# Kernel optimization log

Measured on AMD Instinct MI355X. Metric: run time of the kernel, lower is better.

Reference implementation:

```python
import jax, jax.numpy as jnp
import numpy as np

B, T, D, H = 32, 512, 512, 512  # batch, seq_len, emb dim, lstm_size
TAGS = (17, 9, 25, 13)


def _reverse_sequence(x, lengths):
    # tf.reverse_sequence semantics: reverse first `len` steps, keep the tail.
    t = jnp.arange(x.shape[1])
    idx = jnp.where(t[None, :] < lengths[:, None], lengths[:, None] - 1 - t[None, :], t[None, :])
    return jnp.take_along_axis(x, idx[:, :, None], axis=1)


def _lstm(x, W, b, lengths):
    # TF LSTMCell: kernel [D+H,4H], gate order (i, j, f, o), forget_bias=1.0.
    # dynamic_rnn: state copied through past seq_len, outputs zeroed past seq_len.
    Bx, Tx, _ = x.shape
    Hh = b.shape[-1] // 4
    xT = jnp.swapaxes(x, 0, 1)  # [T,B,D]
    mask = (jnp.arange(Tx)[:, None] < lengths[None, :]).astype(x.dtype)[:, :, None]  # [T,B,1]

    def step(carry, inp):
        c, h = carry
        xt, m = inp
        z = jnp.concatenate([xt, h], axis=-1) @ W + b  # [B,4H]
        i, j, f, o = jnp.split(z, 4, axis=-1)
        c_new = jax.nn.sigmoid(f + 1.0) * c + jax.nn.sigmoid(i) * jnp.tanh(j)
        h_new = jax.nn.sigmoid(o) * jnp.tanh(c_new)
        c = m * c_new + (1.0 - m) * c
        h = m * h_new + (1.0 - m) * h
        return (c, h), h * m

    init = (jnp.zeros((Bx, Hh), x.dtype), jnp.zeros((Bx, Hh), x.dtype))
    _, hs = jax.lax.scan(step, init, (xT, mask))
    return jnp.swapaxes(hs, 0, 1)  # [B,T,H]


def _bilstm(x, lengths, Wf, bf, Wb, bb):
    out_fw = _lstm(x, Wf, bf, lengths)
    x_rev = _reverse_sequence(x, lengths)
    out_bw = _reverse_sequence(_lstm(x_rev, Wb, bb, lengths), lengths)
    return jnp.concatenate([out_fw, out_bw], axis=2)  # [B,T,2H]


def setup_inputs() -> dict:
    key = jax.random.key(0)
    ks = jax.random.split(key, 12)
    s_in = 1.0 / np.sqrt(D + H)
    s_fc = 1.0 / np.sqrt(4 * H)
    inp = {
        'embedded_words': jax.random.normal(ks[0], (B, T, D), jnp.float32),
        'sentence_lengths': jax.random.randint(ks[1], (B,), 16, T + 1, jnp.int32),
        'W_fw': jax.random.normal(ks[2], (5, D + H, 4 * H), jnp.float32) * s_in,
        'b_fw': jnp.zeros((5, 4 * H), jnp.float32),
        'W_bw': jax.random.normal(ks[3], (5, D + H, 4 * H), jnp.float32) * s_in,
        'b_bw': jnp.zeros((5, 4 * H), jnp.float32),
    }
    for i, tg in enumerate(TAGS):
        inp[f'W{i+1}'] = jax.random.normal(ks[4 + i], (4 * H, tg), jnp.float32) * s_fc
        inp[f'b{i+1}'] = jnp.zeros((tg,), jnp.float32)
    return inp


def reference(embedded_words, sentence_lengths, W_fw, b_fw, W_bw, b_bw,
              W1, b1, W2, b2, W3, b3, W4, b4):
    # 5 independent BiLSTMs (task1..4 + shared) over the same input, vmapped over the stack axis.
    outs = jax.vmap(lambda wf, bf, wb, bb: _bilstm(embedded_words, sentence_lengths, wf, bf, wb, bb))(
        W_fw, b_fw, W_bw, b_bw)  # [5,B,T,2H]
    shared = outs[4]
    logits = []
    for i, (Wk, bk) in enumerate(((W1, b1), (W2, b2), (W3, b3), (W4, b4))):
        feat = jnp.concatenate([outs[i], shared], axis=2)  # [B,T,4H]; dropout = identity (inference)
        logits.append(jnp.einsum('btd,dk->btk', feat, Wk) + bk)
    # concatenate the 4 task logit heads along the tag axis: [B,T,sum(TAGS)]
    return jnp.concatenate(logits, axis=2)
```

## Files before the change

### kernel.cpp

```cpp
#include <hip/hip_runtime.h>
#include <cstdint>
#include <cstddef>

#define BB 32
#define TT 512
#define DD 512
#define HH 512
#define FOURH 2048
#define DIRS 10
#define HSZ ((size_t)DIRS * BB * HH)
#define LWPITCH 520
#define SMEM_REC (128 * LWPITCH * 2 + 2 * 2 * 4 * 4 * 64 * 4)

typedef unsigned short u16;
typedef __attribute__((ext_vector_type(8))) short short8;
typedef __attribute__((ext_vector_type(4))) float f32x4;

__device__ __forceinline__ u16 f2b(float f) {
    union { float f; unsigned u; } v; v.f = f;
    unsigned u = v.u;
    u = (u + 0x7FFFu + ((u >> 16) & 1u)) >> 16;
    return (u16)u;
}
__device__ __forceinline__ float b2f(u16 b) {
    union { unsigned u; float f; } v; v.u = ((unsigned)b) << 16;
    return v.f;
}
__device__ __forceinline__ float sigm(float x) { return 1.f / (1.f + __expf(-x)); }
__device__ __forceinline__ float tanh_(float x) { return 1.f - 2.f / (1.f + __expf(2.f * x)); }
__device__ __forceinline__ f32x4 fzero() { f32x4 z = {0.f, 0.f, 0.f, 0.f}; return z; }

__device__ __forceinline__ uint4 load_coh16(const u16* p) {
    uint4 r;
    asm volatile("global_load_dwordx4 %0, %1, off sc0 sc1"
                 : "=v"(r) : "v"(p) : "memory");
    return r;
}

__global__ void k_convx(const float* __restrict__ X, u16* __restrict__ XB) {
    int i = blockIdx.x * 256 + threadIdx.x;
    if (i >= (BB * TT * DD) / 4) return;
    float4 v = ((const float4*)X)[i];
    unsigned lo = (unsigned)f2b(v.x) | ((unsigned)f2b(v.y) << 16);
    unsigned hi = (unsigned)f2b(v.z) | ((unsigned)f2b(v.w) << 16);
    uint2 o; o.x = lo; o.y = hi;
    ((uint2*)XB)[i] = o;
}

__global__ void k_wt(const float* __restrict__ Wf, const float* __restrict__ Wb,
                     u16* __restrict__ WT) {
    int d = blockIdx.z, s = d >> 1;
    const float* src = (d & 1) ? Wb : Wf;
    __shared__ float tile[32][33];
    int tx = threadIdx.x & 31, ty = threadIdx.x >> 5;
    int kt = blockIdx.x, nt = blockIdx.y;
#pragma unroll
    for (int r = 0; r < 4; r++) {
        int k = kt * 32 + ty + r * 8, n = nt * 32 + tx;
        tile[ty + r * 8][tx] = src[((size_t)s * 1024 + k) * 2048 + n];
    }
    __syncthreads();
#pragma unroll
    for (int r = 0; r < 4; r++) {
        int n = nt * 32 + ty + r * 8, k = kt * 32 + tx;
        WT[((size_t)d * 2048 + n) * 1024 + k] = f2b(tile[tx][ty + r * 8]);
    }
}

__global__ void k_wbt(const float* W1, const float* W2, const float* W3, const float* W4,
                      const float* b1, const float* b2, const float* b3, const float* b4,
                      u16* __restrict__ WBT, float* __restrict__ B64) {
    int idx = blockIdx.x * 256 + threadIdx.x;
    const int off[4] = {0, 17, 26, 51};
    const int tg[4]  = {17, 9, 25, 13};
    if (idx < 64) {
        int c = idx;
        int ti = (c < 17) ? 0 : (c < 26) ? 1 : (c < 51) ? 2 : 3;
        const float* bbp[4] = {b1, b2, b3, b4};
        B64[c] = bbp[ti][c - off[ti]];
    }
    if (idx >= 64 * 5120) return;
    int c = idx / 5120, k = idx % 5120;
    int ti = (c < 17) ? 0 : (c < 26) ? 1 : (c < 51) ? 2 : 3;
    const float* Ws[4] = {W1, W2, W3, W4};
    int tag = c - off[ti];
    float v;
    if (k < 4096) {
        int i = k >> 10, kk = k & 1023;
        v = (i == ti) ? Ws[ti][(size_t)kk * tg[ti] + tag] : 0.f;
    } else {
        int kk = k - 4096;
        v = Ws[ti][(size_t)(1024 + kk) * tg[ti] + tag];
    }
    WBT[(size_t)c * 5120 + k] = f2b(v);
}

__global__ __launch_bounds__(512, 2) void k_rec(
    const u16* __restrict__ WT, const u16* __restrict__ XB,
    const float* __restrict__ bfw, const float* __restrict__ bbw,
    u16* __restrict__ Hbuf, float* __restrict__ Cst, u16* __restrict__ OUTS,
    const int* __restrict__ lens, unsigned* __restrict__ ctr)
{
    extern __shared__ char smem[];
    u16* lWx = (u16*)smem;
    float* red = (float*)(smem + 128 * LWPITCH * 2);

    int blk = blockIdx.x, d = blk >> 4, jj = blk & 15;
    int s = d >> 1, isbw = d & 1;
    int tid = threadIdx.x, w = tid >> 6, lane = tid & 63, quad = lane >> 4, l15 = lane & 15;
    int mtile = w & 1, nhalf = (w >> 1) & 1, khalf = w >> 2;

#pragma unroll
    for (int it = 0; it < 16; ++it) {
        int g16 = it * 512 + tid;
        int row = g16 >> 6, c = g16 & 63;
        int n = (row >> 5) * 512 + jj * 32 + (row & 31);
        const u16* src = WT + ((size_t)d * 2048 + n) * 1024 + c * 8;
        *(uint4*)(lWx + row * LWPITCH + c * 8) = *(const uint4*)src;
    }

    short8 Bf[8][4];
#pragma unroll
    for (int ks = 0; ks < 8; ks++) {
        int k0 = khalf * 256 + ks * 32;
#pragma unroll
        for (int g = 0; g < 4; g++) {
            int n = g * 512 + jj * 32 + nhalf * 16 + l15;
            Bf[ks][g] = *(const short8*)(WT + ((size_t)d * 2048 + n) * 1024 + 512 + k0 + quad * 8);
        }
    }

    int bA = mtile * 16 + l15;
    int lbA = lens[bA];
    int ug = jj * 32 + nhalf * 16 + l15;
    const float* bias = (isbw ? bbw : bfw) + (size_t)s * 2048;
    float c_reg[4], hprev[4], bv_r[4];
    int lb_r[4];
    if (khalf == 0) {
#pragma unroll
        for (int g = 0; g < 4; g++) bv_r[g] = bias[g * 512 + ug];
#pragma unroll
        for (int r = 0; r < 4; r++) {
            int b = mtile * 16 + quad * 4 + r;
            lb_r[r] = lens[b];
            c_reg[r] = Cst[((size_t)d * BB + b) * HH + ug];
            hprev[r] = b2f(Hbuf[(size_t)d * BB * HH + (size_t)b * HH + ug]);
        }
    }
    __syncthreads();

    for (int t = 0; t < TT; ++t) {
        const u16* hin = Hbuf + (size_t)(t & 1) * HSZ + (size_t)d * BB * HH;
        u16* hout      = Hbuf + (size_t)((t + 1) & 1) * HSZ + (size_t)d * BB * HH;

        int srcT = isbw ? ((t < lbA) ? (lbA - 1 - t) : t) : t;
        const u16* xrow = XB + ((size_t)bA * TT + srcT) * DD + khalf * 256;
        uint4 xraw[8];
#pragma unroll
        for (int ks = 0; ks < 8; ks++)
            xraw[ks] = *(const uint4*)(xrow + ks * 32 + quad * 8);

        uint4 araw[8];
#pragma unroll
        for (int ks = 0; ks < 8; ks++)
            araw[ks] = load_coh16(hin + (size_t)bA * HH + khalf * 256 + ks * 32 + quad * 8);

        f32x4 acc[4];
#pragma unroll
        for (int g = 0; g < 4; g++) acc[g] = fzero();

#pragma unroll
        for (int ks = 0; ks < 8; ks++) {
            short8 a = *(const short8*)(&xraw[ks]);
#pragma unroll
            for (int g = 0; g < 4; g++) {
                short8 bfr = *(const short8*)(lWx + (g * 32 + nhalf * 16 + l15) * LWPITCH
                                              + khalf * 256 + ks * 32 + quad * 8);
                acc[g] = __builtin_amdgcn_mfma_f32_16x16x32_bf16(a, bfr, acc[g], 0, 0, 0);
            }
        }

        asm volatile("s_waitcnt vmcnt(0)" ::: "memory");
#pragma unroll
        for (int ks = 0; ks < 8; ks++) {
            short8 a = *(const short8*)(&araw[ks]);
#pragma unroll
            for (int g = 0; g < 4; g++)
                acc[g] = __builtin_amdgcn_mfma_f32_16x16x32_bf16(a, Bf[ks][g], acc[g], 0, 0, 0);
        }

        if (khalf == 1) {
#pragma unroll
            for (int g = 0; g < 4; g++)
#pragma unroll
                for (int r = 0; r < 4; r++)
                    red[((((size_t)mtile * 2 + nhalf) * 4 + g) * 4 + r) * 64 + lane] = acc[g][r];
        }
        __syncthreads();
        if (khalf == 0) {
#pragma unroll
            for (int g = 0; g < 4; g++)
#pragma unroll
                for (int r = 0; r < 4; r++)
                    acc[g][r] += red[((((size_t)mtile * 2 + nhalf) * 4 + g) * 4 + r) * 64 + lane];

#pragma unroll
            for (int r = 0; r < 4; r++) {
                int b = mtile * 16 + quad * 4 + r;
                int lb = lb_r[r];
                float zi = acc[0][r] + bv_r[0];
                float zj = acc[1][r] + bv_r[1];
                float zf = acc[2][r] + bv_r[2];
                float zo = acc[3][r] + bv_r[3];
                float cn = sigm(zf + 1.f) * c_reg[r] + sigm(zi) * tanh_(zj);
                float hn = sigm(zo) * tanh_(cn);
                bool act = t < lb;
                if (act) c_reg[r] = cn;
                u16 hv = f2b(act ? hn : hprev[r]);
                hprev[r] = b2f(hv);
                __hip_atomic_store(&hout[(size_t)b * HH + ug], hv,
                                   __ATOMIC_RELAXED, __HIP_MEMORY_SCOPE_AGENT);
                int twr = isbw ? (act ? (lb - 1 - t) : t) : t;
                OUTS[(((size_t)s * BB + b) * TT + twr) * 1024 + isbw * 512 + ug] = f2b(act ? hn : 0.f);
            }
        }

        __syncthreads();
        if (tid == 0) {
            atomicAdd(ctr + d * 16, 1u);
            unsigned target = 16u * (unsigned)(t + 1);
            while (__hip_atomic_load(ctr + d * 16, __ATOMIC_RELAXED, __HIP_MEMORY_SCOPE_AGENT) < target)
                __builtin_amdgcn_s_sleep(1);
        }
        __syncthreads();
    }
}

__global__ __launch_bounds__(256) void k_head(
    const u16* __restrict__ OUTS, const u16* __restrict__ WBT,
    const float* __restrict__ B64, float* __restrict__ OUT)
{
    int tid = threadIdx.x, w = tid >> 6, lane = tid & 63, quad = lane >> 4, l15 = lane & 15;
    int mtile = blockIdx.x * 4 + w, r0 = mtile * 16;
    int row_a = r0 + l15, ba = row_a >> 9, ta = row_a & 511;
    f32x4 acc[4];
#pragma unroll
    for (int ni = 0; ni < 4; ni++) acc[ni] = fzero();

    for (int k0 = 0; k0 < 5120; k0 += 32) {
        int kidx = k0 + quad * 8;
        int blkk = kidx >> 10, kk = kidx & 1023;
        short8 a = *(const short8*)(OUTS + (((size_t)blkk * BB + ba) * TT + ta) * 1024 + kk);
#pragma unroll
        for (int ni = 0; ni < 4; ni++) {
            short8 bf = *(const short8*)(WBT + (size_t)(ni * 16 + l15) * 5120 + kidx);
            acc[ni] = __builtin_amdgcn_mfma_f32_16x16x32_bf16(a, bf, acc[ni], 0, 0, 0);
        }
    }
#pragma unroll
    for (int ni = 0; ni < 4; ni++) {
        int c = ni * 16 + l15;
        float bv = B64[c];
#pragma unroll
        for (int r = 0; r < 4; r++) {
            int row = r0 + quad * 4 + r;
            OUT[(size_t)row * 64 + c] = acc[ni][r] + bv;
        }
    }
}

extern "C" void kernel_launch(void* const* d_in, const int* in_sizes, int n_in,
                              void* d_out, int out_size, void* d_ws, size_t ws_size,
                              hipStream_t stream) {
    const float* X   = (const float*)d_in[0];
    const int* lens  = (const int*)d_in[1];
    const float* Wf  = (const float*)d_in[2];
    const float* bf_ = (const float*)d_in[3];
    const float* Wb  = (const float*)d_in[4];
    const float* bb_ = (const float*)d_in[5];
    const float* W1  = (const float*)d_in[6];
    const float* b1  = (const float*)d_in[7];
    const float* W2  = (const float*)d_in[8];
    const float* b2  = (const float*)d_in[9];
    const float* W3  = (const float*)d_in[10];
    const float* b3  = (const float*)d_in[11];
    const float* W4  = (const float*)d_in[12];
    const float* b4  = (const float*)d_in[13];

    char* ws = (char*)d_ws;
    size_t off = 0;
    auto take = [&](size_t bytes) { size_t o = off; off += (bytes + 255) & ~(size_t)255; return o; };
    size_t wtOff   = take((size_t)DIRS * 2048 * 1024 * 2);
    size_t xbOff   = take((size_t)BB * TT * DD * 2);
    size_t outsOff = take((size_t)5 * BB * TT * 1024 * 2);
    size_t hOff    = take((size_t)2 * HSZ * 2);
    size_t cOff    = take((size_t)HSZ * 4);
    size_t ctrOff  = take((size_t)DIRS * 16 * 4);
    size_t wbtOff  = take((size_t)64 * 5120 * 2);
    size_t b64Off  = take((size_t)64 * 4);

    u16* WT    = (u16*)(ws + wtOff);
    u16* XB    = (u16*)(ws + xbOff);
    u16* OUTS  = (u16*)(ws + outsOff);
    u16* Hbuf  = (u16*)(ws + hOff);
    float* Cst = (float*)(ws + cOff);
    unsigned* CTR = (unsigned*)(ws + ctrOff);
    u16* WBT   = (u16*)(ws + wbtOff);
    float* B64 = (float*)(ws + b64Off);

    hipMemsetAsync(ws + hOff, 0, wbtOff - hOff, stream);

    (void)hipFuncSetAttribute((const void*)k_rec,
                              hipFuncAttributeMaxDynamicSharedMemorySize, SMEM_REC);

    k_convx<<<8192, 256, 0, stream>>>(X, XB);
    k_wt<<<dim3(32, 64, 10), 256, 0, stream>>>(Wf, Wb, WT);
    k_wbt<<<1280, 256, 0, stream>>>(W1, W2, W3, W4, b1, b2, b3, b4, WBT, B64);

    k_rec<<<160, 512, SMEM_REC, stream>>>(WT, XB, bf_, bb_, Hbuf, Cst, OUTS, lens, CTR);

    k_head<<<256, 256, 0, stream>>>(OUTS, WBT, B64, (float*)d_out);
}
```

Baseline: 3.692 ms.

## Replace per-step grid barrier with per-wave producer flags and prefetch next x row

Swaps the per-direction atomic counter barrier (two block-wide syncs plus one spinning thread) for per-wave flag words. Each producing wave publishes its timestep after its h stores drain, and each consumer wave polls only the 32 flags covering the h slice it reads. The x input row for the next step is also prefetched at the end of each iteration, so that load overlaps the wait. This cuts the cost of the serial dependency at each timestep, but adds more polling traffic and depends on relaxed-store ordering after vmcnt(0).

```diff
diff --git a/kernel.cpp b/kernel.cpp
--- a/kernel.cpp
+++ b/kernel.cpp
@@ -33,6 +33,12 @@
 __device__ __forceinline__ uint4 load_coh16(const u16* p) {
     uint4 r;
     asm volatile("global_load_dwordx4 %0, %1, off sc0 sc1"
+                 : "=v"(r) : "v"(p) : "memory");
+    return r;
+}
+__device__ __forceinline__ uint4 load_p16(const u16* p) {
+    uint4 r;
+    asm volatile("global_load_dwordx4 %0, %1, off"
                  : "=v"(r) : "v"(p) : "memory");
     return r;
 }
@@ -99,7 +105,7 @@
     const u16* __restrict__ WT, const u16* __restrict__ XB,
     const float* __restrict__ bfw, const float* __restrict__ bbw,
     u16* __restrict__ Hbuf, float* __restrict__ Cst, u16* __restrict__ OUTS,
-    const int* __restrict__ lens, unsigned* __restrict__ ctr)
+    const int* __restrict__ lens, unsigned* __restrict__ flg)
 {
     extern __shared__ char smem[];
     u16* lWx = (u16*)smem;
@@ -147,23 +153,45 @@
             hprev[r] = b2f(Hbuf[(size_t)d * BB * HH + (size_t)b * HH + ug]);
         }
     }
+
+    unsigned* FLG = flg + d * 64;
+    const unsigned* myfl = FLG + khalf * 32;
+    int myflag = jj * 4 + mtile * 2 + nhalf;
+
     __syncthreads();
+
+    uint4 xraw[8];
+    {
+        int srcT = isbw ? (lbA - 1) : 0;
+        const u16* xrow = XB + ((size_t)bA * TT + srcT) * DD + khalf * 256;
+#pragma unroll
+        for (int ks = 0; ks < 8; ks++)
+            xraw[ks] = load_p16(xrow + ks * 32 + quad * 8);
+    }
 
     for (int t = 0; t < TT; ++t) {
         const u16* hin = Hbuf + (size_t)(t & 1) * HSZ + (size_t)d * BB * HH;
         u16* hout      = Hbuf + (size_t)((t + 1) & 1) * HSZ + (size_t)d * BB * HH;
 
-        int srcT = isbw ? ((t < lbA) ? (lbA - 1 - t) : t) : t;
-        const u16* xrow = XB + ((size_t)bA * TT + srcT) * DD + khalf * 256;
-        uint4 xraw[8];
-#pragma unroll
-        for (int ks = 0; ks < 8; ks++)
-            xraw[ks] = *(const uint4*)(xrow + ks * 32 + quad * 8);
+        if (t > 0) {
+            unsigned tgt = (unsigned)t;
+            for (;;) {
+                unsigned f = tgt;
+                if (lane < 32)
+                    f = __hip_atomic_load(myfl + lane, __ATOMIC_RELAXED,
+                                          __HIP_MEMORY_SCOPE_AGENT);
+                if (__all((int)(f >= tgt))) break;
+                __builtin_amdgcn_s_sleep(1);
+            }
+        }
 
         uint4 araw[8];
 #pragma unroll
         for (int ks = 0; ks < 8; ks++)
             araw[ks] = load_coh16(hin + (size_t)bA * HH + khalf * 256 + ks * 32 + quad * 8);
+
+        asm volatile("s_waitcnt vmcnt(8)" ::: "memory");
+        __builtin_amdgcn_sched_barrier(0);
 
         f32x4 acc[4];
 #pragma unroll
@@ -181,6 +209,7 @@
         }
 
         asm volatile("s_waitcnt vmcnt(0)" ::: "memory");
+        __builtin_amdgcn_sched_barrier(0);
 #pragma unroll
         for (int ks = 0; ks < 8; ks++) {
             short8 a = *(const short8*)(&araw[ks]);
@@ -189,6 +218,7 @@
                 acc[g] = __builtin_amdgcn_mfma_f32_16x16x32_bf16(a, Bf[ks][g], acc[g], 0, 0, 0);
         }
 
+        __syncthreads();
         if (khalf == 1) {
 #pragma unroll
             for (int g = 0; g < 4; g++)
@@ -223,16 +253,19 @@
                 int twr = isbw ? (act ? (lb - 1 - t) : t) : t;
                 OUTS[(((size_t)s * BB + b) * TT + twr) * 1024 + isbw * 512 + ug] = f2b(act ? hn : 0.f);
             }
-        }
-
-        __syncthreads();
-        if (tid == 0) {
-            atomicAdd(ctr + d * 16, 1u);
-            unsigned target = 16u * (unsigned)(t + 1);
-            while (__hip_atomic_load(ctr + d * 16, __ATOMIC_RELAXED, __HIP_MEMORY_SCOPE_AGENT) < target)
-                __builtin_amdgcn_s_sleep(1);
-        }
-        __syncthreads();
+            asm volatile("s_waitcnt vmcnt(0)" ::: "memory");
+            __builtin_amdgcn_sched_barrier(0);
+            if (lane == 0)
+                __hip_atomic_store(FLG + myflag, (unsigned)(t + 1),
+                                   __ATOMIC_RELAXED, __HIP_MEMORY_SCOPE_AGENT);
+        }
+
+        int tn = (t + 1 < TT) ? (t + 1) : (TT - 1);
+        int srcTn = isbw ? ((tn < lbA) ? (lbA - 1 - tn) : tn) : tn;
+        const u16* xrown = XB + ((size_t)bA * TT + srcTn) * DD + khalf * 256;
+#pragma unroll
+        for (int ks = 0; ks < 8; ks++)
+            xraw[ks] = load_p16(xrown + ks * 32 + quad * 8);
     }
 }
 
@@ -295,7 +328,7 @@
     size_t outsOff = take((size_t)5 * BB * TT * 1024 * 2);
     size_t hOff    = take((size_t)2 * HSZ * 2);
     size_t cOff    = take((size_t)HSZ * 4);
-    size_t ctrOff  = take((size_t)DIRS * 16 * 4);
+    size_t flgOff  = take((size_t)DIRS * 64 * 4);
     size_t wbtOff  = take((size_t)64 * 5120 * 2);
     size_t b64Off  = take((size_t)64 * 4);
 
@@ -304,7 +337,7 @@
     u16* OUTS  = (u16*)(ws + outsOff);
     u16* Hbuf  = (u16*)(ws + hOff);
     float* Cst = (float*)(ws + cOff);
-    unsigned* CTR = (unsigned*)(ws + ctrOff);
+    unsigned* FLG = (unsigned*)(ws + flgOff);
     u16* WBT   = (u16*)(ws + wbtOff);
     float* B64 = (float*)(ws + b64Off);
 
@@ -317,7 +350,7 @@
     k_wt<<<dim3(32, 64, 10), 256, 0, stream>>>(Wf, Wb, WT);
     k_wbt<<<1280, 256, 0, stream>>>(W1, W2, W3, W4, b1, b2, b3, b4, WBT, B64);
 
-    k_rec<<<160, 512, SMEM_REC, stream>>>(WT, XB, bf_, bb_, Hbuf, Cst, OUTS, lens, CTR);
+    k_rec<<<160, 512, SMEM_REC, stream>>>(WT, XB, bf_, bb_, Hbuf, Cst, OUTS, lens, FLG);
 
     k_head<<<256, 256, 0, stream>>>(OUTS, WBT, B64, (float*)d_out);
 }
```

Measured after the change: 4.041 ms. +9.5%, slower.

## Interleave fwd/bwd directions per block with per-block flag barriers

Applied to the files above, without the earlier changes.

Each block now owns 16 hidden units for both the forward and the backward direction of one stack and alternates between them within each time step. While one direction waits on its cross-block dependency, the other direction's work can proceed. The single atomic counter barrier is replaced by per-block step flags that a wavefront polls in parallel, and the other direction's flags are prefetched. The gate reduction and cell update are spread across all 512 threads with a padded LDS layout. The change adds complexity, a bounded spin loop, and a relaxed-ordering flag protocol that could race.

```diff
diff --git a/kernel.cpp b/kernel.cpp
--- a/kernel.cpp
+++ b/kernel.cpp
@@ -6,11 +6,11 @@
 #define TT 512
 #define DD 512
 #define HH 512
-#define FOURH 2048
 #define DIRS 10
 #define HSZ ((size_t)DIRS * BB * HH)
 #define LWPITCH 520
-#define SMEM_REC (128 * LWPITCH * 2 + 2 * 2 * 4 * 4 * 64 * 4)
+#define REDPITCH 66
+#define SMEM_REC (128 * LWPITCH * 2 + 64 * REDPITCH * 4)
 
 typedef unsigned short u16;
 typedef __attribute__((ext_vector_type(8))) short short8;
@@ -98,141 +98,155 @@
 __global__ __launch_bounds__(512, 2) void k_rec(
     const u16* __restrict__ WT, const u16* __restrict__ XB,
     const float* __restrict__ bfw, const float* __restrict__ bbw,
-    u16* __restrict__ Hbuf, float* __restrict__ Cst, u16* __restrict__ OUTS,
-    const int* __restrict__ lens, unsigned* __restrict__ ctr)
+    u16* __restrict__ Hbuf, u16* __restrict__ OUTS,
+    const int* __restrict__ lens, unsigned* __restrict__ flg)
 {
     extern __shared__ char smem[];
     u16* lWx = (u16*)smem;
     float* red = (float*)(smem + 128 * LWPITCH * 2);
 
-    int blk = blockIdx.x, d = blk >> 4, jj = blk & 15;
-    int s = d >> 1, isbw = d & 1;
+    int blk = blockIdx.x, s = blk >> 5, jj = blk & 31, d0 = s * 2;
     int tid = threadIdx.x, w = tid >> 6, lane = tid & 63, quad = lane >> 4, l15 = lane & 15;
-    int mtile = w & 1, nhalf = (w >> 1) & 1, khalf = w >> 2;
+    int gsel = w & 1, mtile = (w >> 1) & 1, khalf = w >> 2;
 
 #pragma unroll
     for (int it = 0; it < 16; ++it) {
         int g16 = it * 512 + tid;
         int row = g16 >> 6, c = g16 & 63;
-        int n = (row >> 5) * 512 + jj * 32 + (row & 31);
-        const u16* src = WT + ((size_t)d * 2048 + n) * 1024 + c * 8;
+        int dq = row >> 6, local = row & 63;
+        int n = (local >> 4) * 512 + jj * 16 + (local & 15);
+        const u16* src = WT + ((size_t)(d0 + dq) * 2048 + n) * 1024 + c * 8;
         *(uint4*)(lWx + row * LWPITCH + c * 8) = *(const uint4*)src;
     }
 
-    short8 Bf[8][4];
-#pragma unroll
-    for (int ks = 0; ks < 8; ks++) {
-        int k0 = khalf * 256 + ks * 32;
-#pragma unroll
-        for (int g = 0; g < 4; g++) {
-            int n = g * 512 + jj * 32 + nhalf * 16 + l15;
-            Bf[ks][g] = *(const short8*)(WT + ((size_t)d * 2048 + n) * 1024 + 512 + k0 + quad * 8);
-        }
-    }
+    short8 Bf[2][8][2];
+#pragma unroll
+    for (int dd = 0; dd < 2; dd++)
+#pragma unroll
+        for (int ks = 0; ks < 8; ks++)
+#pragma unroll
+            for (int gb = 0; gb < 2; gb++) {
+                int n = (gsel * 2 + gb) * 512 + jj * 16 + l15;
+                int k = 512 + khalf * 256 + ks * 32 + quad * 8;
+                Bf[dd][ks][gb] = *(const short8*)(WT + ((size_t)(d0 + dd) * 2048 + n) * 1024 + k);
+            }
 
     int bA = mtile * 16 + l15;
     int lbA = lens[bA];
-    int ug = jj * 32 + nhalf * 16 + l15;
-    const float* bias = (isbw ? bbw : bfw) + (size_t)s * 2048;
-    float c_reg[4], hprev[4], bv_r[4];
-    int lb_r[4];
-    if (khalf == 0) {
-#pragma unroll
-        for (int g = 0; g < 4; g++) bv_r[g] = bias[g * 512 + ug];
-#pragma unroll
-        for (int r = 0; r < 4; r++) {
-            int b = mtile * 16 + quad * 4 + r;
-            lb_r[r] = lens[b];
-            c_reg[r] = Cst[((size_t)d * BB + b) * HH + ug];
-            hprev[r] = b2f(Hbuf[(size_t)d * BB * HH + (size_t)b * HH + ug]);
+    int cb = tid >> 4, cu = tid & 15;
+    int lbC = lens[cb];
+    int myq = (cb >> 2) & 3, myr = cb & 3, mym = cb >> 4;
+    float cst[2] = {0.f, 0.f}, hpv[2] = {0.f, 0.f};
+    float bv[2][4];
+#pragma unroll
+    for (int dd = 0; dd < 2; dd++) {
+        const float* bias = (dd ? bbw : bfw) + (size_t)s * 2048;
+#pragma unroll
+        for (int g4 = 0; g4 < 4; g4++) bv[dd][g4] = bias[g4 * 512 + jj * 16 + cu];
+    }
+
+    unsigned fpre = 0;
+
+    __syncthreads();
+
+    for (int t = 0; t < TT; ++t) {
+#pragma unroll
+        for (int dd = 0; dd < 2; ++dd) {
+            int d = d0 + dd;
+            unsigned tgt = (unsigned)t;
+
+            if (!__all((int)(fpre >= tgt))) {
+                const unsigned* fp = flg + (size_t)d * 64;
+                for (int spin = 0; spin < (1 << 21); ++spin) {
+                    unsigned f = 0xFFFFFFFFu;
+                    if (lane < 32)
+                        f = __hip_atomic_load(fp + lane, __ATOMIC_RELAXED,
+                                              __HIP_MEMORY_SCOPE_AGENT);
+                    if (__all((int)(f >= tgt))) break;
+                    __builtin_amdgcn_s_sleep(2);
+                }
+            }
+
+            int srcT = dd ? ((t < lbA) ? (lbA - 1 - t) : t) : t;
+            const u16* xrow = XB + ((size_t)bA * TT + srcT) * DD + khalf * 256;
+            uint4 xraw[8];
+#pragma unroll
+            for (int ks = 0; ks < 8; ks++)
+                xraw[ks] = *(const uint4*)(xrow + ks * 32 + quad * 8);
+
+            const u16* hin = Hbuf + (size_t)(t & 1) * HSZ + (size_t)d * BB * HH;
+            uint4 araw[8];
+#pragma unroll
+            for (int ks = 0; ks < 8; ks++)
+                araw[ks] = load_coh16(hin + (size_t)bA * HH + khalf * 256 + ks * 32 + quad * 8);
+
+            f32x4 acc[2];
+            acc[0] = fzero(); acc[1] = fzero();
+
+#pragma unroll
+            for (int ks = 0; ks < 8; ks++) {
+                short8 a = *(const short8*)(&xraw[ks]);
+#pragma unroll
+                for (int gb = 0; gb < 2; gb++) {
+                    int row = dd * 64 + (gsel * 2 + gb) * 16 + l15;
+                    short8 bfr = *(const short8*)(lWx + row * LWPITCH
+                                                  + khalf * 256 + ks * 32 + quad * 8);
+                    acc[gb] = __builtin_amdgcn_mfma_f32_16x16x32_bf16(a, bfr, acc[gb], 0, 0, 0);
+                }
+            }
+
+            asm volatile("s_waitcnt vmcnt(0)" ::: "memory");
+            __builtin_amdgcn_sched_barrier(0);
+#pragma unroll
+            for (int ks = 0; ks < 8; ks++) {
+                short8 a = *(const short8*)(&araw[ks]);
+#pragma unroll
+                for (int gb = 0; gb < 2; gb++)
+                    acc[gb] = __builtin_amdgcn_mfma_f32_16x16x32_bf16(a, Bf[dd][ks][gb], acc[gb], 0, 0, 0);
+            }
+
+#pragma unroll
+            for (int gb = 0; gb < 2; gb++)
+#pragma unroll
+                for (int r = 0; r < 4; r++) {
+                    int R = (((khalf * 2 + gsel) * 2 + gb) * 2 + mtile) * 4 + r;
+                    red[R * REDPITCH + lane] = acc[gb][r];
+                }
+            __syncthreads();
+
+            float z[4];
+#pragma unroll
+            for (int g4 = 0; g4 < 4; g4++) {
+                int gs = g4 >> 1, gb = g4 & 1;
+                int R0 = (((0 * 2 + gs) * 2 + gb) * 2 + mym) * 4 + myr;
+                int R1 = (((1 * 2 + gs) * 2 + gb) * 2 + mym) * 4 + myr;
+                z[g4] = red[R0 * REDPITCH + myq * 16 + cu]
+                      + red[R1 * REDPITCH + myq * 16 + cu] + bv[dd][g4];
+            }
+            float cn = sigm(z[2] + 1.f) * cst[dd] + sigm(z[0]) * tanh_(z[1]);
+            float hn = sigm(z[3]) * tanh_(cn);
+            bool act = t < lbC;
+            if (act) cst[dd] = cn;
+            u16 hv = f2b(act ? hn : hpv[dd]);
+            hpv[dd] = b2f(hv);
+            u16* hout = Hbuf + (size_t)((t + 1) & 1) * HSZ + (size_t)d * BB * HH;
+            __hip_atomic_store(&hout[(size_t)cb * HH + jj * 16 + cu], hv,
+                               __ATOMIC_RELAXED, __HIP_MEMORY_SCOPE_AGENT);
+            int twr = dd ? (act ? (lbC - 1 - t) : t) : t;
+            OUTS[(((size_t)s * BB + cb) * TT + twr) * 1024 + dd * 512 + jj * 16 + cu]
+                = f2b(act ? hn : 0.f);
+
+            int ndd = dd ^ 1;
+            fpre = 0xFFFFFFFFu;
+            if (lane < 32)
+                fpre = __hip_atomic_load(flg + (size_t)(d0 + ndd) * 64 + lane,
+                                         __ATOMIC_RELAXED, __HIP_MEMORY_SCOPE_AGENT);
+
+            __syncthreads();
+            if (tid == 0)
+                __hip_atomic_store(flg + (size_t)d * 64 + jj, (unsigned)(t + 1),
+                                   __ATOMIC_RELAXED, __HIP_MEMORY_SCOPE_AGENT);
         }
-    }
-    __syncthreads();
-
-    for (int t = 0; t < TT; ++t) {
-        const u16* hin = Hbuf + (size_t)(t & 1) * HSZ + (size_t)d * BB * HH;
-        u16* hout      = Hbuf + (size_t)((t + 1) & 1) * HSZ + (size_t)d * BB * HH;
-
-        int srcT = isbw ? ((t < lbA) ? (lbA - 1 - t) : t) : t;
-        const u16* xrow = XB + ((size_t)bA * TT + srcT) * DD + khalf * 256;
-        uint4 xraw[8];
-#pragma unroll
-        for (int ks = 0; ks < 8; ks++)
-            xraw[ks] = *(const uint4*)(xrow + ks * 32 + quad * 8);
-
-        uint4 araw[8];
-#pragma unroll
-        for (int ks = 0; ks < 8; ks++)
-            araw[ks] = load_coh16(hin + (size_t)bA * HH + khalf * 256 + ks * 32 + quad * 8);
-
-        f32x4 acc[4];
-#pragma unroll
-        for (int g = 0; g < 4; g++) acc[g] = fzero();
-
-#pragma unroll
-        for (int ks = 0; ks < 8; ks++) {
-            short8 a = *(const short8*)(&xraw[ks]);
-#pragma unroll
-            for (int g = 0; g < 4; g++) {
-                short8 bfr = *(const short8*)(lWx + (g * 32 + nhalf * 16 + l15) * LWPITCH
-                                              + khalf * 256 + ks * 32 + quad * 8);
-                acc[g] = __builtin_amdgcn_mfma_f32_16x16x32_bf16(a, bfr, acc[g], 0, 0, 0);
-            }
-        }
-
-        asm volatile("s_waitcnt vmcnt(0)" ::: "memory");
-#pragma unroll
-        for (int ks = 0; ks < 8; ks++) {
-            short8 a = *(const short8*)(&araw[ks]);
-#pragma unroll
-            for (int g = 0; g < 4; g++)
-                acc[g] = __builtin_amdgcn_mfma_f32_16x16x32_bf16(a, Bf[ks][g], acc[g], 0, 0, 0);
-        }
-
-        if (khalf == 1) {
-#pragma unroll
-            for (int g = 0; g < 4; g++)
-#pragma unroll
-                for (int r = 0; r < 4; r++)
-                    red[((((size_t)mtile * 2 + nhalf) * 4 + g) * 4 + r) * 64 + lane] = acc[g][r];
-        }
-        __syncthreads();
-        if (khalf == 0) {
-#pragma unroll
-            for (int g = 0; g < 4; g++)
-#pragma unroll
-                for (int r = 0; r < 4; r++)
-                    acc[g][r] += red[((((size_t)mtile * 2 + nhalf) * 4 + g) * 4 + r) * 64 + lane];
-
-#pragma unroll
-            for (int r = 0; r < 4; r++) {
-                int b = mtile * 16 + quad * 4 + r;
-                int lb = lb_r[r];
-                float zi = acc[0][r] + bv_r[0];
-                float zj = acc[1][r] + bv_r[1];
-                float zf = acc[2][r] + bv_r[2];
-                float zo = acc[3][r] + bv_r[3];
-                float cn = sigm(zf + 1.f) * c_reg[r] + sigm(zi) * tanh_(zj);
-                float hn = sigm(zo) * tanh_(cn);
-                bool act = t < lb;
-                if (act) c_reg[r] = cn;
-                u16 hv = f2b(act ? hn : hprev[r]);
-                hprev[r] = b2f(hv);
-                __hip_atomic_store(&hout[(size_t)b * HH + ug], hv,
-                                   __ATOMIC_RELAXED, __HIP_MEMORY_SCOPE_AGENT);
-                int twr = isbw ? (act ? (lb - 1 - t) : t) : t;
-                OUTS[(((size_t)s * BB + b) * TT + twr) * 1024 + isbw * 512 + ug] = f2b(act ? hn : 0.f);
-            }
-        }
-
-        __syncthreads();
-        if (tid == 0) {
-            atomicAdd(ctr + d * 16, 1u);
-            unsigned target = 16u * (unsigned)(t + 1);
-            while (__hip_atomic_load(ctr + d * 16, __ATOMIC_RELAXED, __HIP_MEMORY_SCOPE_AGENT) < target)
-                __builtin_amdgcn_s_sleep(1);
-        }
-        __syncthreads();
     }
 }
 
@@ -294,8 +308,7 @@
     size_t xbOff   = take((size_t)BB * TT * DD * 2);
     size_t outsOff = take((size_t)5 * BB * TT * 1024 * 2);
     size_t hOff    = take((size_t)2 * HSZ * 2);
-    size_t cOff    = take((size_t)HSZ * 4);
-    size_t ctrOff  = take((size_t)DIRS * 16 * 4);
+    size_t flgOff  = take((size_t)DIRS * 64 * 4);
     size_t wbtOff  = take((size_t)64 * 5120 * 2);
     size_t b64Off  = take((size_t)64 * 4);
 
@@ -303,8 +316,7 @@
     u16* XB    = (u16*)(ws + xbOff);
     u16* OUTS  = (u16*)(ws + outsOff);
     u16* Hbuf  = (u16*)(ws + hOff);
-    float* Cst = (float*)(ws + cOff);
-    unsigned* CTR = (unsigned*)(ws + ctrOff);
+    unsigned* FLG = (unsigned*)(ws + flgOff);
     u16* WBT   = (u16*)(ws + wbtOff);
     float* B64 = (float*)(ws + b64Off);
 
@@ -317,7 +329,7 @@
     k_wt<<<dim3(32, 64, 10), 256, 0, stream>>>(Wf, Wb, WT);
     k_wbt<<<1280, 256, 0, stream>>>(W1, W2, W3, W4, b1, b2, b3, b4, WBT, B64);
 
-    k_rec<<<160, 512, SMEM_REC, stream>>>(WT, XB, bf_, bb_, Hbuf, Cst, OUTS, lens, CTR);
+    k_rec<<<160, 512, SMEM_REC, stream>>>(WT, XB, bf_, bb_, Hbuf, OUTS, lens, FLG);
 
     k_head<<<256, 256, 0, stream>>>(OUTS, WBT, B64, (float*)d_out);
 }
```

After: 5.147 ms. 39.4% more time.

## Replace per-step counter barrier with step-tagged hidden-state words and triple buffering

Applied to the files above, without the earlier changes.

Each hidden-state bf16 value is now stored as a 32-bit word tagged with the timestep in its upper half, in a triple-buffered array. Consumers spin-load their own slice until every tag matches the expected step. This replaces the global atomic counter barrier and its extra __syncthreads. The change removes a serialized atomic round-trip per step and lets blocks proceed once their specific inputs are ready. In exchange, the hidden-state read traffic doubles, the polling loop is bounded, and correctness depends on the tag protocol and the third buffer slot.

```diff
diff --git a/kernel.cpp b/kernel.cpp
--- a/kernel.cpp
+++ b/kernel.cpp
@@ -6,11 +6,10 @@
 #define TT 512
 #define DD 512
 #define HH 512
-#define FOURH 2048
 #define DIRS 10
-#define HSZ ((size_t)DIRS * BB * HH)
 #define LWPITCH 520
 #define SMEM_REC (128 * LWPITCH * 2 + 2 * 2 * 4 * 4 * 64 * 4)
+#define HB32SZ ((size_t)3 * DIRS * BB * HH)
 
 typedef unsigned short u16;
 typedef __attribute__((ext_vector_type(8))) short short8;
@@ -30,11 +29,13 @@
 __device__ __forceinline__ float tanh_(float x) { return 1.f - 2.f / (1.f + __expf(2.f * x)); }
 __device__ __forceinline__ f32x4 fzero() { f32x4 z = {0.f, 0.f, 0.f, 0.f}; return z; }
 
-__device__ __forceinline__ uint4 load_coh16(const u16* p) {
-    uint4 r;
-    asm volatile("global_load_dwordx4 %0, %1, off sc0 sc1"
-                 : "=v"(r) : "v"(p) : "memory");
-    return r;
+__device__ __forceinline__ short8 pk2(uint4 a, uint4 b) {
+    union { unsigned d[4]; short8 s; } u;
+    u.d[0] = (a.x & 0xFFFFu) | (a.y << 16);
+    u.d[1] = (a.z & 0xFFFFu) | (a.w << 16);
+    u.d[2] = (b.x & 0xFFFFu) | (b.y << 16);
+    u.d[3] = (b.z & 0xFFFFu) | (b.w << 16);
+    return u.s;
 }
 
 __global__ void k_convx(const float* __restrict__ X, u16* __restrict__ XB) {
@@ -98,8 +99,8 @@
 __global__ __launch_bounds__(512, 2) void k_rec(
     const u16* __restrict__ WT, const u16* __restrict__ XB,
     const float* __restrict__ bfw, const float* __restrict__ bbw,
-    u16* __restrict__ Hbuf, float* __restrict__ Cst, u16* __restrict__ OUTS,
-    const int* __restrict__ lens, unsigned* __restrict__ ctr)
+    unsigned* __restrict__ Hb32, u16* __restrict__ OUTS,
+    const int* __restrict__ lens)
 {
     extern __shared__ char smem[];
     u16* lWx = (u16*)smem;
@@ -143,16 +144,13 @@
         for (int r = 0; r < 4; r++) {
             int b = mtile * 16 + quad * 4 + r;
             lb_r[r] = lens[b];
-            c_reg[r] = Cst[((size_t)d * BB + b) * HH + ug];
-            hprev[r] = b2f(Hbuf[(size_t)d * BB * HH + (size_t)b * HH + ug]);
+            c_reg[r] = 0.f;
+            hprev[r] = 0.f;
         }
     }
     __syncthreads();
 
     for (int t = 0; t < TT; ++t) {
-        const u16* hin = Hbuf + (size_t)(t & 1) * HSZ + (size_t)d * BB * HH;
-        u16* hout      = Hbuf + (size_t)((t + 1) & 1) * HSZ + (size_t)d * BB * HH;
-
         int srcT = isbw ? ((t < lbA) ? (lbA - 1 - t) : t) : t;
         const u16* xrow = XB + ((size_t)bA * TT + srcT) * DD + khalf * 256;
         uint4 xraw[8];
@@ -160,10 +158,50 @@
         for (int ks = 0; ks < 8; ks++)
             xraw[ks] = *(const uint4*)(xrow + ks * 32 + quad * 8);
 
-        uint4 araw[8];
-#pragma unroll
-        for (int ks = 0; ks < 8; ks++)
-            araw[ks] = load_coh16(hin + (size_t)bA * HH + khalf * 256 + ks * 32 + quad * 8);
+        int sl = t % 3;
+        const unsigned* hb = Hb32 + (((size_t)sl * DIRS + d) * BB + bA) * HH
+                             + khalf * 256 + quad * 8;
+        unsigned exp_ = ((unsigned)t) << 16;
+        uint4 p0, p1, p2, p3, p4, p5, p6, p7, p8, p9, pA, pB, pC, pD, pE, pF;
+        for (int spin = 0; spin < (1 << 16); ++spin) {
+            asm volatile(
+                "global_load_dwordx4 %0, %16, off sc0 sc1\n\t"
+                "global_load_dwordx4 %1, %16, off offset:16 sc0 sc1\n\t"
+                "global_load_dwordx4 %2, %16, off offset:128 sc0 sc1\n\t"
+                "global_load_dwordx4 %3, %16, off offset:144 sc0 sc1\n\t"
+                "global_load_dwordx4 %4, %16, off offset:256 sc0 sc1\n\t"
+                "global_load_dwordx4 %5, %16, off offset:272 sc0 sc1\n\t"
+                "global_load_dwordx4 %6, %16, off offset:384 sc0 sc1\n\t"
+                "global_load_dwordx4 %7, %16, off offset:400 sc0 sc1\n\t"
+                "global_load_dwordx4 %8, %16, off offset:512 sc0 sc1\n\t"
+                "global_load_dwordx4 %9, %16, off offset:528 sc0 sc1\n\t"
+                "global_load_dwordx4 %10, %16, off offset:640 sc0 sc1\n\t"
+                "global_load_dwordx4 %11, %16, off offset:656 sc0 sc1\n\t"
+                "global_load_dwordx4 %12, %16, off offset:768 sc0 sc1\n\t"
+                "global_load_dwordx4 %13, %16, off offset:784 sc0 sc1\n\t"
+                "global_load_dwordx4 %14, %16, off offset:896 sc0 sc1\n\t"
+                "global_load_dwordx4 %15, %16, off offset:912 sc0 sc1\n\t"
+                "s_waitcnt vmcnt(0)"
+                : "=&v"(p0), "=&v"(p1), "=&v"(p2), "=&v"(p3),
+                  "=&v"(p4), "=&v"(p5), "=&v"(p6), "=&v"(p7),
+                  "=&v"(p8), "=&v"(p9), "=&v"(pA), "=&v"(pB),
+                  "=&v"(pC), "=&v"(pD), "=&v"(pE), "=&v"(pF)
+                : "v"(hb) : "memory");
+#define TB_(P) ((P.x ^ exp_) | (P.y ^ exp_) | (P.z ^ exp_) | (P.w ^ exp_))
+            unsigned bad = TB_(p0) | TB_(p1) | TB_(p2) | TB_(p3)
+                         | TB_(p4) | TB_(p5) | TB_(p6) | TB_(p7)
+                         | TB_(p8) | TB_(p9) | TB_(pA) | TB_(pB)
+                         | TB_(pC) | TB_(pD) | TB_(pE) | TB_(pF);
+#undef TB_
+            if (__all((int)((bad >> 16) == 0u))) break;
+            __builtin_amdgcn_s_sleep(1);
+        }
+
+        short8 Af[8];
+        Af[0] = pk2(p0, p1); Af[1] = pk2(p2, p3);
+        Af[2] = pk2(p4, p5); Af[3] = pk2(p6, p7);
+        Af[4] = pk2(p8, p9); Af[5] = pk2(pA, pB);
+        Af[6] = pk2(pC, pD); Af[7] = pk2(pE, pF);
 
         f32x4 acc[4];
 #pragma unroll
@@ -179,14 +217,11 @@
                 acc[g] = __builtin_amdgcn_mfma_f32_16x16x32_bf16(a, bfr, acc[g], 0, 0, 0);
             }
         }
-
-        asm volatile("s_waitcnt vmcnt(0)" ::: "memory");
 #pragma unroll
         for (int ks = 0; ks < 8; ks++) {
-            short8 a = *(const short8*)(&araw[ks]);
 #pragma unroll
             for (int g = 0; g < 4; g++)
-                acc[g] = __builtin_amdgcn_mfma_f32_16x16x32_bf16(a, Bf[ks][g], acc[g], 0, 0, 0);
+                acc[g] = __builtin_amdgcn_mfma_f32_16x16x32_bf16(Af[ks], Bf[ks][g], acc[g], 0, 0, 0);
         }
 
         if (khalf == 1) {
@@ -204,6 +239,9 @@
                 for (int r = 0; r < 4; r++)
                     acc[g][r] += red[((((size_t)mtile * 2 + nhalf) * 4 + g) * 4 + r) * 64 + lane];
 
+            unsigned tg1 = ((unsigned)(t + 1)) << 16;
+            int sl1 = (t + 1) % 3;
+            unsigned* hout = Hb32 + ((size_t)sl1 * DIRS + d) * BB * HH;
 #pragma unroll
             for (int r = 0; r < 4; r++) {
                 int b = mtile * 16 + quad * 4 + r;
@@ -218,19 +256,11 @@
                 if (act) c_reg[r] = cn;
                 u16 hv = f2b(act ? hn : hprev[r]);
                 hprev[r] = b2f(hv);
-                __hip_atomic_store(&hout[(size_t)b * HH + ug], hv,
+                __hip_atomic_store(&hout[(size_t)b * HH + ug], tg1 | (unsigned)hv,
                                    __ATOMIC_RELAXED, __HIP_MEMORY_SCOPE_AGENT);
                 int twr = isbw ? (act ? (lb - 1 - t) : t) : t;
                 OUTS[(((size_t)s * BB + b) * TT + twr) * 1024 + isbw * 512 + ug] = f2b(act ? hn : 0.f);
             }
-        }
-
-        __syncthreads();
-        if (tid == 0) {
-            atomicAdd(ctr + d * 16, 1u);
-            unsigned target = 16u * (unsigned)(t + 1);
-            while (__hip_atomic_load(ctr + d * 16, __ATOMIC_RELAXED, __HIP_MEMORY_SCOPE_AGENT) < target)
-                __builtin_amdgcn_s_sleep(1);
         }
         __syncthreads();
     }
@@ -293,22 +323,18 @@
     size_t wtOff   = take((size_t)DIRS * 2048 * 1024 * 2);
     size_t xbOff   = take((size_t)BB * TT * DD * 2);
     size_t outsOff = take((size_t)5 * BB * TT * 1024 * 2);
-    size_t hOff    = take((size_t)2 * HSZ * 2);
-    size_t cOff    = take((size_t)HSZ * 4);
-    size_t ctrOff  = take((size_t)DIRS * 16 * 4);
+    size_t hbOff   = take(HB32SZ * 4);
     size_t wbtOff  = take((size_t)64 * 5120 * 2);
     size_t b64Off  = take((size_t)64 * 4);
 
     u16* WT    = (u16*)(ws + wtOff);
     u16* XB    = (u16*)(ws + xbOff);
     u16* OUTS  = (u16*)(ws + outsOff);
-    u16* Hbuf  = (u16*)(ws + hOff);
-    float* Cst = (float*)(ws + cOff);
-    unsigned* CTR = (unsigned*)(ws + ctrOff);
+    unsigned* HB32 = (unsigned*)(ws + hbOff);
     u16* WBT   = (u16*)(ws + wbtOff);
     float* B64 = (float*)(ws + b64Off);
 
-    hipMemsetAsync(ws + hOff, 0, wbtOff - hOff, stream);
+    hipMemsetAsync(ws + hbOff, 0, HB32SZ * 4, stream);
 
     (void)hipFuncSetAttribute((const void*)k_rec,
                               hipFuncAttributeMaxDynamicSharedMemorySize, SMEM_REC);
@@ -317,7 +343,7 @@
     k_wt<<<dim3(32, 64, 10), 256, 0, stream>>>(Wf, Wb, WT);
     k_wbt<<<1280, 256, 0, stream>>>(W1, W2, W3, W4, b1, b2, b3, b4, WBT, B64);
 
-    k_rec<<<160, 512, SMEM_REC, stream>>>(WT, XB, bf_, bb_, Hbuf, Cst, OUTS, lens, CTR);
+    k_rec<<<160, 512, SMEM_REC, stream>>>(WT, XB, bf_, bb_, HB32, OUTS, lens);
 
     k_head<<<256, 256, 0, stream>>>(OUTS, WBT, B64, (float*)d_out);
 }
```

New measurement: 8.084 ms. +119.0%, slower.
